# Kernel tuning notes

Hardware: AMD Instinct MI355X
Metric: run time of the kernel (lower is better)

Reference implementation:

```python
import jax, jax.numpy as jnp
import numpy as np

B, T, H, L, AS = 64, 256, 1024, 3, 128  # batch, seq-1, hidden, layers, alphabet


def setup_inputs() -> dict:
    key = jax.random.key(0)
    ks = jax.random.split(key, 8)
    # one-hot character sequence (B, T, AS), float32
    idx = jax.random.randint(ks[0], (B, T), 0, AS)
    sequence = jax.nn.one_hot(idx, AS, dtype=jnp.float32)
    u = lambda k, shape, fan: jax.random.uniform(
        k, shape, minval=-1.0 / np.sqrt(fan), maxval=1.0 / np.sqrt(fan), dtype=jnp.float32)
    W_i2h = u(ks[1], (H, AS), AS)
    b_i2h = u(ks[2], (H,), AS)
    # per-layer LSTM params, PyTorch gate order [i, f, g, o]; layer inputs all have width H
    W_ih = u(ks[3], (L, 4 * H, H), H)
    W_hh = u(ks[4], (L, 4 * H, H), H)
    b_ih = u(ks[5], (L, 4 * H), H)
    b_hh = u(ks[6], (L, 4 * H), H)
    W_h2O = u(ks[7], (AS, H), H)
    b_h2O = jnp.zeros((AS,), dtype=jnp.float32)
    h0 = jnp.zeros((L, B, H), dtype=jnp.float32)
    c0 = jnp.zeros((L, B, H), dtype=jnp.float32)
    return dict(sequence=sequence, W_i2h=W_i2h, b_i2h=b_i2h, W_ih=W_ih, W_hh=W_hh,
                b_ih=b_ih, b_hh=b_hh, W_h2O=W_h2O, b_h2O=b_h2O, h0=h0, c0=c0)


def _lstm_layer(x, h0, c0, W_ih, W_hh, b_ih, b_hh):
    # x: (B, T, H). Precompute input contribution to the gates for all steps.
    xg = jnp.einsum('bth,gh->btg', x, W_ih) + b_ih  # (B, T, 4H)

    def step(carry, xg_t):
        h, c = carry
        gates = xg_t + h @ W_hh.T + b_hh  # (B, 4H)
        i, f, g, o = jnp.split(gates, 4, axis=-1)
        c = jax.nn.sigmoid(f) * c + jax.nn.sigmoid(i) * jnp.tanh(g)
        h = jax.nn.sigmoid(o) * jnp.tanh(c)
        return (h, c), h

    (hT, cT), hs = jax.lax.scan(step, (h0, c0), jnp.swapaxes(xg, 0, 1))
    return jnp.swapaxes(hs, 0, 1), hT, cT  # (B,T,H), (B,H), (B,H)


def reference(sequence, W_i2h, b_i2h, W_ih, W_hh, b_ih, b_hh, W_h2O, b_h2O, h0, c0):
    # i2h projection
    x = jnp.einsum('bta,ha->bth', sequence, W_i2h) + b_i2h  # (B, T, H)
    # multi-layer LSTM over x (eval mode: the dropout=True arg is inactive in eval)
    inp = x
    h_fin, c_fin = [], []
    for l in range(L):
        inp, hT, cT = _lstm_layer(inp, h0[l], c0[l], W_ih[l], W_hh[l], b_ih[l], b_hh[l])
        h_fin.append(hT)
        c_fin.append(cT)
    # NOTE: faithful to the original code's bug -- h2O is applied to the i2h
    # output `x`, not to the LSTM output. The LSTM only produces the new hidden.
    out = x.reshape(-1, H) @ W_h2O.T + b_h2O  # (B*T, AS)
    return out, jnp.stack(h_fin), jnp.stack(c_fin)
```

## Files before the change

kernel.cpp:

```cpp
#include <hip/hip_runtime.h>
#include <stdint.h>
#include <stddef.h>

#define B_  64
#define T_  256
#define H_  1024
#define AS_ 128
#define L_  3

typedef __attribute__((ext_vector_type(8))) short bf16x8;
typedef __attribute__((ext_vector_type(4))) float f32x4;
typedef __attribute__((ext_vector_type(4))) unsigned u32x4;

__device__ __forceinline__ unsigned short f2bf(float f) {
  union { float f; unsigned u; } x; x.f = f;
  unsigned r = x.u + 0x7fffu + ((x.u >> 16) & 1u);
  return (unsigned short)(r >> 16);
}
__device__ __forceinline__ float bf2f(unsigned short s) {
  union { unsigned u; float f; } x; x.u = ((unsigned)s) << 16; return x.f;
}
__device__ __forceinline__ float sigmf(float x) { return 1.0f / (1.0f + __expf(-x)); }
__device__ __forceinline__ float tanh_f(float x) {
  x = fminf(fmaxf(x, -15.0f), 15.0f);
  float e = __expf(2.0f * x);
  return (e - 1.0f) / (e + 1.0f);
}

__device__ __forceinline__ void st_u16_cc(unsigned short* p, unsigned short v) {
  __hip_atomic_store(p, v, __ATOMIC_RELAXED, __HIP_MEMORY_SCOPE_AGENT);
}
__device__ __forceinline__ void st_u32_cc(unsigned* p, unsigned v) {
  __hip_atomic_store(p, v, __ATOMIC_RELAXED, __HIP_MEMORY_SCOPE_AGENT);
}
__device__ __forceinline__ unsigned ld_u32_cc(const unsigned* p) {
  return __hip_atomic_load(p, __ATOMIC_RELAXED, __HIP_MEMORY_SCOPE_AGENT);
}
__device__ __forceinline__ u32x4 ld_b128_cc_nw(const void* p) {
  u32x4 r;
  asm volatile("global_load_dwordx4 %0, %1, off sc0 sc1" : "=v"(r) : "v"(p));
  return r;
}
__device__ __forceinline__ void st_b128_cc_nw(void* p, u32x4 v) {
  asm volatile("global_store_dwordx4 %0, %1, off sc0 sc1" :: "v"(p), "v"(v) : "memory");
}
__device__ __forceinline__ void wait_vm4_tie4(u32x4& a, u32x4& b, u32x4& c, u32x4& d) {
  asm volatile("s_waitcnt vmcnt(4)"
               : "+v"(a), "+v"(b), "+v"(c), "+v"(d) :: "memory");
  __builtin_amdgcn_sched_barrier(0);
}
__device__ __forceinline__ void wait_vm0_tie4(u32x4& a, u32x4& b, u32x4& c, u32x4& d) {
  asm volatile("s_waitcnt vmcnt(0)"
               : "+v"(a), "+v"(b), "+v"(c), "+v"(d) :: "memory");
  __builtin_amdgcn_sched_barrier(0);
}
__device__ __forceinline__ void lds_barrier() {
  __builtin_amdgcn_sched_barrier(0);
  asm volatile("s_waitcnt lgkmcnt(0)" ::: "memory");
  __builtin_amdgcn_sched_barrier(0);
  __builtin_amdgcn_s_barrier();
  __builtin_amdgcn_sched_barrier(0);
}


__global__ void k_zero(unsigned* p, int n) {
  int i = blockIdx.x * 256 + threadIdx.x;
  if (i < n) st_u32_cc(p + i, 0u);
}

__global__ void k_wt_i2h(const float* __restrict__ W, const float* __restrict__ b,
                         unsigned short* __restrict__ Wt) {
  int id = blockIdx.x * 256 + threadIdx.x;
  if (id >= AS_ * H_) return;
  int a = id >> 10, h = id & 1023;
  Wt[id] = f2bf(W[h * AS_ + a] + b[h]);
}

__global__ void k_f2b(const float* __restrict__ s, unsigned short* __restrict__ d, int n) {
  int i = blockIdx.x * 256 + threadIdx.x;
  if (i < n) d[i] = f2bf(s[i]);
}

__global__ void k_bias(const float* __restrict__ bi, const float* __restrict__ bh,
                       float* __restrict__ o, int n) {
  int i = blockIdx.x * 256 + threadIdx.x;
  if (i < n) o[i] = bi[i] + bh[i];
}

__global__ __launch_bounds__(128) void k_gather(const float* __restrict__ seq,
                                                const unsigned short* __restrict__ Wt,
                                                unsigned short* __restrict__ xbf) {
  __shared__ int sidx;
  const int bt = blockIdx.x, tid = threadIdx.x;
  if (seq[(size_t)bt * AS_ + tid] > 0.5f) sidx = tid;
  __syncthreads();
  const uint4* s = (const uint4*)(Wt + (size_t)sidx * H_);
  uint4* d = (uint4*)(xbf + (size_t)bt * H_);
  d[tid] = s[tid];
}


__device__ __forceinline__ void gld16(const void* g, void* l) {
  __builtin_amdgcn_global_load_lds((const __attribute__((address_space(1))) unsigned int*)g,
                                   (__attribute__((address_space(3))) unsigned int*)l,
                                   16, 0, 0);
}

template <int OUT, int AMAJ>
__device__ __forceinline__ void gemm_tile(const unsigned short* __restrict__ A,
                                          const unsigned short* __restrict__ Bm,
                                          const float* __restrict__ bias,
                                          void* __restrict__ Cout,
                                          int m0, int n0, int K, int N, int tid,
                                          unsigned short* As, unsigned short* Bs) {
  const int lane = tid & 63, wv = tid >> 6;
  const int wr = wv >> 1, wc = wv & 1;
  const int kg = lane >> 4, li = lane & 15;
  f32x4 acc[4][4] = {};

  for (int k0 = 0; k0 < K; k0 += 32) {
    for (int i = 0; i < 2; ++i) {
      int c0 = i * 256 + wv * 64;
      int cid = c0 + lane;
      int row = cid >> 2, lc = cid & 3;
      int sc = lc ^ ((row >> 1) & 3);
      gld16(A + (size_t)(m0 + row) * K + k0 + sc * 8, (char*)As + (size_t)c0 * 16);
      gld16(Bm + (size_t)(n0 + row) * K + k0 + sc * 8, (char*)Bs + (size_t)c0 * 16);
    }
    __syncthreads();
    bf16x8 af[4], bfm[4];
#pragma unroll
    for (int mi = 0; mi < 4; ++mi) {
      int row = wr * 64 + mi * 16 + li;
      int pc = kg ^ ((row >> 1) & 3);
      af[mi] = *(const bf16x8*)((const char*)As + row * 64 + pc * 16);
    }
#pragma unroll
    for (int ni = 0; ni < 4; ++ni) {
      int row = wc * 64 + ni * 16 + li;
      int pc = kg ^ ((row >> 1) & 3);
      bfm[ni] = *(const bf16x8*)((const char*)Bs + row * 64 + pc * 16);
    }
#pragma unroll
    for (int mi = 0; mi < 4; ++mi)
#pragma unroll
      for (int ni = 0; ni < 4; ++ni)
        acc[mi][ni] = __builtin_amdgcn_mfma_f32_16x16x32_bf16(af[mi], bfm[ni], acc[mi][ni], 0, 0, 0);
    __syncthreads();
  }

#pragma unroll
  for (int mi = 0; mi < 4; ++mi)
#pragma unroll
    for (int ni = 0; ni < 4; ++ni)
#pragma unroll
      for (int r = 0; r < 4; ++r) {
        int row = m0 + wr * 64 + mi * 16 + kg * 4 + r;
        int col = n0 + wc * 64 + ni * 16 + li;
        float v = acc[mi][ni][r] + bias[col];
        if (OUT == 0) {
          ((float*)Cout)[(size_t)row * N + col] = v;
        } else {
          int b, tt;
          if (AMAJ == 0) { b = row >> 8; tt = row & 255; }
          else           { tt = row >> 6; b = row & 63; }
          int g = col >> 10, u = col & 1023;
          int idx = ((tt * 4 + (b >> 4)) << 16) | ((u >> 5) << 11) |
                    ((b & 15) << 7) | ((u & 31) << 2) | g;
          ((unsigned short*)Cout)[idx] = f2bf(v);
        }
      }
}

template <int OUT, int AMAJ>
__global__ __launch_bounds__(256) void k_gemm(const unsigned short* __restrict__ A,
                                              const unsigned short* __restrict__ Bm,
                                              const float* __restrict__ bias,
                                              void* __restrict__ Cout,
                                              int M, int N, int K) {
  __shared__ __align__(16) unsigned short As[128 * 32];
  __shared__ __align__(16) unsigned short Bs[128 * 32];
  gemm_tile<OUT, AMAJ>(A, Bm, bias, Cout, blockIdx.x * 128, blockIdx.y * 128,
                       K, N, threadIdx.x, As, Bs);
}


__global__ __launch_bounds__(256, 1) void k_fused(
    const unsigned short* __restrict__ xgs,
    const float* __restrict__ Whh,
    unsigned short* __restrict__ h_pp,
    unsigned short* __restrict__ out_seq,
    float* __restrict__ hT, float* __restrict__ cT,
    const float* __restrict__ h0, const float* __restrict__ c0,
    unsigned* __restrict__ slots,
    const unsigned short* __restrict__ WihbN,
    const float* __restrict__ bsumN,
    unsigned short* __restrict__ xgs_out) {
  __shared__ __align__(16) unsigned short Wlds[64 * 1024];
  __shared__ __align__(16) unsigned short Hs[16 * 1024];
  const int tid = threadIdx.x, lane = tid & 63, w = tid >> 6;
  const int wg = blockIdx.x;

  if (wg >= 128) {
    const int Wp = wg - 128;
    unsigned short* As = Wlds;
    unsigned short* Bs = Wlds + 4096;
    const int pline = (Wp & 31) * 32;
    for (int k = 0; k < 32; ++k) {
      const int gidx = Wp + k * 128;
      const int mt = gidx >> 5, nt = gidx & 31;
      const unsigned tgt = (unsigned)(2 * mt + 3);
      if (w == 0) {
        const unsigned* base = slots + (lane >> 4) * 1024 + pline + (lane & 15);
        unsigned v0, v1;
        do {
          __builtin_amdgcn_s_sleep(4);
          v0 = ld_u32_cc(base);
          v1 = ld_u32_cc(base + 16);
        } while (__any((int)((v0 < tgt) | (v1 < tgt))));
      }
      __syncthreads();
      gemm_tile<2, 1>(out_seq, WihbN, bsumN, (void*)xgs_out,
                      mt * 128, nt * 128, H_, 4 * H_, tid, As, Bs);
    }
    return;
  }

  const int gb = wg >> 5, ug = wg & 31;
  const int li = lane & 15, kq = lane >> 4;
  const int b  = gb * 16 + li;
  const int u0 = ug * 32 + w * 8 + kq;
  const int u1 = u0 + 4;

  st_u16_cc(&h_pp[((size_t)B_ + b) * H_ + u0], f2bf(h0[(size_t)b * H_ + u0]));
  st_u16_cc(&h_pp[((size_t)B_ + b) * H_ + u1], f2bf(h0[(size_t)b * H_ + u1]));

  bf16x8 afr[32];
  {
    const int r0 = w * 32 + li;
    const float* wr = Whh + ((size_t)(r0 & 3) * H_ + ug * 32 + (r0 >> 2)) * H_ + kq * 8;
#pragma unroll
    for (int ks = 0; ks < 32; ++ks) {
      const float4 f0 = *(const float4*)(wr + ks * 32);
      const float4 f1 = *(const float4*)(wr + ks * 32 + 4);
      union { ushort4 a[2]; bf16x8 v; } uu_;
      uu_.a[0] = ushort4{f2bf(f0.x), f2bf(f0.y), f2bf(f0.z), f2bf(f0.w)};
      uu_.a[1] = ushort4{f2bf(f1.x), f2bf(f1.y), f2bf(f1.z), f2bf(f1.w)};
      afr[ks] = uu_.v;
    }
  }
  for (int it = 0; it < 16; ++it) {
    const int r = w * 32 + 16 + it;
    const float* wr = Whh + ((size_t)(r & 3) * H_ + ug * 32 + (r >> 2)) * H_;
#pragma unroll
    for (int j = 0; j < 4; ++j) {
      const float4 f = *(const float4*)(wr + lane * 16 + j * 4);
      ushort4 p = ushort4{f2bf(f.x), f2bf(f.y), f2bf(f.z), f2bf(f.w)};
      const int k = lane * 16 + j * 4;
      *(ushort4*)((char*)Wlds + (size_t)(w * 16 + it) * 2048 + ((2 * k) ^ ((it & 7) << 4))) = p;
    }
  }
  float cs0 = c0[(size_t)b * H_ + u0], cs1 = c0[(size_t)b * H_ + u1];
  __syncthreads();
  if (w == 3 && lane < 32) {
    st_u32_cc(&slots[gb * 1024 + lane * 32 + ug], 1u);
    asm volatile("s_waitcnt vmcnt(0)" ::: "memory");
  }

  const char* hbase = (const char*)Hs + (size_t)li * 2048;
  const char* wlb   = (const char*)Wlds + (size_t)(w * 16 + li) * 2048;
  const int fxor = (li & 7) << 4;
  const int sb = tid >> 4, seg = tid & 15;
  const int sswz = (sb & 7) << 4;
  char* drow = (char*)Hs + (size_t)sb * 2048;
  unsigned short* exch = Hs;
  const unsigned* myline = slots + gb * 1024 + ug * 32;

  for (int t = 0; t < T_; ++t) {
    const size_t xb2 = ((((size_t)t * 4 + gb) << 16) | (ug << 11) | (li << 7) |
                        ((w * 8 + kq) << 2)) * 2;
    const ushort4 xa = *(const ushort4*)((const char*)xgs + xb2);
    const ushort4 xb = *(const ushort4*)((const char*)xgs + xb2 + 32);

    if (w == 0) {
      const unsigned tgt = (unsigned)(t + 1);
      unsigned v;
      do {
        __builtin_amdgcn_s_sleep(1);
        v = ld_u32_cc(&myline[lane & 31]);
      } while (__any((int)(v < tgt)));
    }
    __syncthreads();

    const char* srcrow = (const char*)(h_pp + (size_t)((t & 1) ^ 1) * (B_ * H_) +
                                       (size_t)(gb * 16 + sb) * H_);
    u32x4 A0 = ld_b128_cc_nw(srcrow +   0 * 256 + seg * 16);
    u32x4 A1 = ld_b128_cc_nw(srcrow +   1 * 256 + seg * 16);
    u32x4 A2 = ld_b128_cc_nw(srcrow +   2 * 256 + seg * 16);
    u32x4 A3 = ld_b128_cc_nw(srcrow +   3 * 256 + seg * 16);
    u32x4 B0 = ld_b128_cc_nw(srcrow + 1024 + 0 * 256 + seg * 16);
    u32x4 B1 = ld_b128_cc_nw(srcrow + 1024 + 1 * 256 + seg * 16);
    u32x4 B2 = ld_b128_cc_nw(srcrow + 1024 + 2 * 256 + seg * 16);
    u32x4 B3 = ld_b128_cc_nw(srcrow + 1024 + 3 * 256 + seg * 16);
    wait_vm4_tie4(A0, A1, A2, A3);
    *(u32x4*)(drow + ((0 * 256 + seg * 16) ^ sswz)) = A0;
    *(u32x4*)(drow + ((1 * 256 + seg * 16) ^ sswz)) = A1;
    *(u32x4*)(drow + ((2 * 256 + seg * 16) ^ sswz)) = A2;
    *(u32x4*)(drow + ((3 * 256 + seg * 16) ^ sswz)) = A3;
    lds_barrier();

    f32x4 a0 = {0.f, 0.f, 0.f, 0.f}, a1 = {0.f, 0.f, 0.f, 0.f};
#pragma unroll
    for (int ks = 0; ks < 16; ++ks) {
      const bf16x8 bb = *(const bf16x8*)(hbase + ((ks * 64 + kq * 16) ^ fxor));
      a0 = __builtin_amdgcn_mfma_f32_16x16x32_bf16(afr[ks], bb, a0, 0, 0, 0);
      const bf16x8 aw = *(const bf16x8*)(wlb + ((ks * 64 + kq * 16) ^ fxor));
      a1 = __builtin_amdgcn_mfma_f32_16x16x32_bf16(aw, bb, a1, 0, 0, 0);
    }

    wait_vm0_tie4(B0, B1, B2, B3);
    *(u32x4*)(drow + ((1024 + 0 * 256 + seg * 16) ^ sswz)) = B0;
    *(u32x4*)(drow + ((1024 + 1 * 256 + seg * 16) ^ sswz)) = B1;
    *(u32x4*)(drow + ((1024 + 2 * 256 + seg * 16) ^ sswz)) = B2;
    *(u32x4*)(drow + ((1024 + 3 * 256 + seg * 16) ^ sswz)) = B3;
    lds_barrier();

#pragma unroll
    for (int ks = 16; ks < 32; ++ks) {
      const bf16x8 bb = *(const bf16x8*)(hbase + ((ks * 64 + kq * 16) ^ fxor));
      a0 = __builtin_amdgcn_mfma_f32_16x16x32_bf16(afr[ks], bb, a0, 0, 0, 0);
      const bf16x8 aw = *(const bf16x8*)(wlb + ((ks * 64 + kq * 16) ^ fxor));
      a1 = __builtin_amdgcn_mfma_f32_16x16x32_bf16(aw, bb, a1, 0, 0, 0);
    }

    float h0v, h1v;
    {
      float gi = a0[0] + bf2f(xa.x), gf = a0[1] + bf2f(xa.y);
      float gg = a0[2] + bf2f(xa.z), go = a0[3] + bf2f(xa.w);
      float ci = sigmf(gf) * cs0 + sigmf(gi) * tanh_f(gg);
      cs0 = ci; h0v = sigmf(go) * tanh_f(ci);
    }
    {
      float gi = a1[0] + bf2f(xb.x), gf = a1[1] + bf2f(xb.y);
      float gg = a1[2] + bf2f(xb.z), go = a1[3] + bf2f(xb.w);
      float ci = sigmf(gf) * cs1 + sigmf(gi) * tanh_f(gg);
      cs1 = ci; h1v = sigmf(go) * tanh_f(ci);
    }
    const unsigned short hb0 = f2bf(h0v), hb1 = f2bf(h1v);

    __syncthreads();
    exch[li * 32 + w * 8 + kq]     = hb0;
    exch[li * 32 + w * 8 + kq + 4] = hb1;
    __syncthreads();

    if (t < T_ - 1) {
      const int bl = tid >> 4, j = tid & 15;
      const unsigned pack = (unsigned)exch[bl * 32 + 2 * j] |
                            ((unsigned)exch[bl * 32 + 2 * j + 1] << 16);
      st_u32_cc((unsigned*)&h_pp[((size_t)(t & 1) * B_ + gb * 16 + bl) * H_ + ug * 32 + 2 * j],
                pack);
    } else {
      hT[(size_t)b * H_ + u0] = h0v; hT[(size_t)b * H_ + u1] = h1v;
      cT[(size_t)b * H_ + u0] = cs0; cT[(size_t)b * H_ + u1] = cs1;
    }
    if (out_seq && tid < 64) {
      const int bo = tid >> 2, q = tid & 3;
      st_b128_cc_nw(&out_seq[((size_t)t * B_ + gb * 16 + bo) * H_ + ug * 32 + 8 * q],
                    *(const u32x4*)&exch[bo * 32 + 8 * q]);
    }
    asm volatile("s_waitcnt vmcnt(0)" ::: "memory");
    __syncthreads();
    if (w == 3 && lane < 32) {
      st_u32_cc(&slots[gb * 1024 + lane * 32 + ug], (unsigned)(t + 2));
      asm volatile("s_waitcnt vmcnt(0)" ::: "memory");
    }
  }
}


extern "C" void kernel_launch(void* const* d_in, const int* in_sizes, int n_in,
                              void* d_out, int out_size, void* d_ws, size_t ws_size,
                              hipStream_t stream) {
  const float* seq  = (const float*)d_in[0];
  const float* Wi2h = (const float*)d_in[1];
  const float* bi2h = (const float*)d_in[2];
  const float* Wih  = (const float*)d_in[3];
  const float* Whh  = (const float*)d_in[4];
  const float* bih  = (const float*)d_in[5];
  const float* bhh  = (const float*)d_in[6];
  const float* Wh2o = (const float*)d_in[7];
  const float* bh2o = (const float*)d_in[8];
  const float* h0   = (const float*)d_in[9];
  const float* c0   = (const float*)d_in[10];
  float* outF = (float*)d_out;

  size_t off = 0;
  auto nb = [&](size_t bytes) { size_t r = off; off += (bytes + 255) & ~(size_t)255; return r; };
  unsigned short* xbf   = (unsigned short*)((char*)d_ws + nb((size_t)B_ * T_ * H_ * 2));
  unsigned short* seqA  = (unsigned short*)((char*)d_ws + nb((size_t)B_ * T_ * H_ * 2));
  unsigned short* xgs   = (unsigned short*)((char*)d_ws + nb((size_t)B_ * T_ * 4 * H_ * 2));
  unsigned short* Wihb  = (unsigned short*)((char*)d_ws + nb((size_t)L_ * 4 * H_ * H_ * 2));
  unsigned short* Wh2ob = (unsigned short*)((char*)d_ws + nb((size_t)AS_ * H_ * 2));
  unsigned short* Wt    = (unsigned short*)((char*)d_ws + nb((size_t)AS_ * H_ * 2));
  float*          bsum  = (float*)((char*)d_ws + nb((size_t)L_ * 4 * H_ * 4));
  unsigned short* h_pp  = (unsigned short*)((char*)d_ws + nb((size_t)2 * B_ * H_ * 2));
  unsigned*       slt   = (unsigned*)((char*)d_ws + nb((size_t)L_ * 4 * 32 * 32 * 4));
  (void)ws_size; (void)in_sizes; (void)n_in; (void)out_size;

  const int WLAYER = 4 * H_ * H_;

  k_zero<<<(L_ * 4096 + 255) / 256, 256, 0, stream>>>(slt, L_ * 4096);
  k_wt_i2h<<<(AS_ * H_ + 255) / 256, 256, 0, stream>>>(Wi2h, bi2h, Wt);
  k_f2b<<<(L_ * WLAYER + 255) / 256, 256, 0, stream>>>(Wih, Wihb, L_ * WLAYER);
  k_f2b<<<(AS_ * H_ + 255) / 256, 256, 0, stream>>>(Wh2o, Wh2ob, AS_ * H_);
  k_bias<<<(L_ * 4 * H_ + 255) / 256, 256, 0, stream>>>(bih, bhh, bsum, L_ * 4 * H_);
  k_gather<<<B_ * T_, 128, 0, stream>>>(seq, Wt, xbf);

  k_gemm<0, 0><<<dim3(B_ * T_ / 128, AS_ / 128), 256, 0, stream>>>(
      xbf, Wh2ob, bh2o, (void*)outF, B_ * T_, AS_, H_);

  k_gemm<2, 0><<<dim3(B_ * T_ / 128, 4 * H_ / 128), 256, 0, stream>>>(
      xbf, Wihb, bsum, (void*)xgs, B_ * T_, 4 * H_, H_);

  float* hT_base = outF + (size_t)B_ * T_ * AS_;
  float* cT_base = hT_base + (size_t)L_ * B_ * H_;

  k_fused<<<256, 256, 0, stream>>>(
      xgs, Whh, h_pp, seqA,
      hT_base, cT_base, h0, c0, slt,
      Wihb + (size_t)1 * WLAYER, bsum + (size_t)1 * 4 * H_, xgs);

  k_fused<<<256, 256, 0, stream>>>(
      xgs, Whh + (size_t)1 * WLAYER, h_pp, xbf,
      hT_base + (size_t)B_ * H_, cT_base + (size_t)B_ * H_,
      h0 + (size_t)B_ * H_, c0 + (size_t)B_ * H_, slt + (size_t)4096,
      Wihb + (size_t)2 * WLAYER, bsum + (size_t)2 * 4 * H_, xgs);

  k_fused<<<128, 256, 0, stream>>>(
      xgs, Whh + (size_t)2 * WLAYER, h_pp, nullptr,
      hT_base + (size_t)2 * B_ * H_, cT_base + (size_t)2 * B_ * H_,
      h0 + (size_t)2 * B_ * H_, c0 + (size_t)2 * B_ * H_, slt + (size_t)2 * 4096,
      nullptr, nullptr, nullptr);
}
```

Measured before the change: 3.488 ms.

## Fold layer-0 input GEMM and output projection into fused recurrent kernel with progress flags

The standalone layer-0 input-projection GEMM and the h2O output GEMM are removed and run inside the first fused LSTM kernel's spare worker blocks. Those blocks publish per-tile progress counters, and the recurrent blocks poll them before reading each timestep's gate inputs. The gather writes x in time-major order to match, and five small prep kernels are merged into one launch. The aim is to overlap the big input GEMM with the sequential recurrence and cut launch overhead. In exchange it adds polling cost, coherent loads on the gate-input path, and a risk of contention between the GEMM blocks and the recurrent ones.

```diff
diff --git a/kernel.cpp b/kernel.cpp
--- a/kernel.cpp
+++ b/kernel.cpp
@@ -41,12 +41,18 @@
   asm volatile("global_load_dwordx4 %0, %1, off sc0 sc1" : "=v"(r) : "v"(p));
   return r;
 }
+__device__ __forceinline__ unsigned long long ld_b64_cc_nw(const void* p) {
+  unsigned long long r;
+  asm volatile("global_load_dwordx2 %0, %1, off sc0 sc1" : "=v"(r) : "v"(p));
+  return r;
+}
 __device__ __forceinline__ void st_b128_cc_nw(void* p, u32x4 v) {
   asm volatile("global_store_dwordx4 %0, %1, off sc0 sc1" :: "v"(p), "v"(v) : "memory");
 }
-__device__ __forceinline__ void wait_vm4_tie4(u32x4& a, u32x4& b, u32x4& c, u32x4& d) {
+__device__ __forceinline__ void wait_vm4_tie6(u32x4& a, u32x4& b, u32x4& c, u32x4& d,
+                                              unsigned long long& x, unsigned long long& y) {
   asm volatile("s_waitcnt vmcnt(4)"
-               : "+v"(a), "+v"(b), "+v"(c), "+v"(d) :: "memory");
+               : "+v"(a), "+v"(b), "+v"(c), "+v"(d), "+v"(x), "+v"(y) :: "memory");
   __builtin_amdgcn_sched_barrier(0);
 }
 __device__ __forceinline__ void wait_vm0_tie4(u32x4& a, u32x4& b, u32x4& c, u32x4& d) {
@@ -63,28 +69,23 @@
 }
 
 
-__global__ void k_zero(unsigned* p, int n) {
+__global__ void k_prep(unsigned* __restrict__ zp, int nzero,
+                       const float* __restrict__ Wi2h, const float* __restrict__ bi2h,
+                       unsigned short* __restrict__ Wt,
+                       const float* __restrict__ Wih, unsigned short* __restrict__ Wihb, int nwih,
+                       const float* __restrict__ Wh2o, unsigned short* __restrict__ Wh2ob,
+                       const float* __restrict__ bih, const float* __restrict__ bhh,
+                       float* __restrict__ bsum) {
   int i = blockIdx.x * 256 + threadIdx.x;
-  if (i < n) st_u32_cc(p + i, 0u);
-}
-
-__global__ void k_wt_i2h(const float* __restrict__ W, const float* __restrict__ b,
-                         unsigned short* __restrict__ Wt) {
-  int id = blockIdx.x * 256 + threadIdx.x;
-  if (id >= AS_ * H_) return;
-  int a = id >> 10, h = id & 1023;
-  Wt[id] = f2bf(W[h * AS_ + a] + b[h]);
-}
-
-__global__ void k_f2b(const float* __restrict__ s, unsigned short* __restrict__ d, int n) {
-  int i = blockIdx.x * 256 + threadIdx.x;
-  if (i < n) d[i] = f2bf(s[i]);
-}
-
-__global__ void k_bias(const float* __restrict__ bi, const float* __restrict__ bh,
-                       float* __restrict__ o, int n) {
-  int i = blockIdx.x * 256 + threadIdx.x;
-  if (i < n) o[i] = bi[i] + bh[i];
+  if (i < nzero) { st_u32_cc(zp + i, 0u); return; }
+  i -= nzero;
+  if (i < AS_ * H_) { int a = i >> 10, h = i & 1023; Wt[i] = f2bf(Wi2h[h * AS_ + a] + bi2h[h]); return; }
+  i -= AS_ * H_;
+  if (i < nwih) { Wihb[i] = f2bf(Wih[i]); return; }
+  i -= nwih;
+  if (i < AS_ * H_) { Wh2ob[i] = f2bf(Wh2o[i]); return; }
+  i -= AS_ * H_;
+  if (i < L_ * 4 * H_) bsum[i] = bih[i] + bhh[i];
 }
 
 __global__ __launch_bounds__(128) void k_gather(const float* __restrict__ seq,
@@ -94,8 +95,9 @@
   const int bt = blockIdx.x, tid = threadIdx.x;
   if (seq[(size_t)bt * AS_ + tid] > 0.5f) sidx = tid;
   __syncthreads();
+  const int b = bt >> 8, t = bt & 255;
   const uint4* s = (const uint4*)(Wt + (size_t)sidx * H_);
-  uint4* d = (uint4*)(xbf + (size_t)bt * H_);
+  uint4* d = (uint4*)(xbf + ((size_t)t * B_ + b) * H_);
   d[tid] = s[tid];
 }
 
@@ -106,7 +108,7 @@
                                    16, 0, 0);
 }
 
-template <int OUT, int AMAJ>
+template <int OUT>
 __device__ __forceinline__ void gemm_tile(const unsigned short* __restrict__ A,
                                           const unsigned short* __restrict__ Bm,
                                           const float* __restrict__ bias,
@@ -158,30 +160,17 @@
         int row = m0 + wr * 64 + mi * 16 + kg * 4 + r;
         int col = n0 + wc * 64 + ni * 16 + li;
         float v = acc[mi][ni][r] + bias[col];
-        if (OUT == 0) {
-          ((float*)Cout)[(size_t)row * N + col] = v;
+        int tt = row >> 6, b = row & 63;
+        if (OUT == 4) {
+          ((float*)Cout)[(size_t)(b * 256 + tt) * N + col] = v;
         } else {
-          int b, tt;
-          if (AMAJ == 0) { b = row >> 8; tt = row & 255; }
-          else           { tt = row >> 6; b = row & 63; }
           int g = col >> 10, u = col & 1023;
           int idx = ((tt * 4 + (b >> 4)) << 16) | ((u >> 5) << 11) |
                     ((b & 15) << 7) | ((u & 31) << 2) | g;
-          ((unsigned short*)Cout)[idx] = f2bf(v);
+          if (OUT == 3) st_u16_cc(&((unsigned short*)Cout)[idx], f2bf(v));
+          else          ((unsigned short*)Cout)[idx] = f2bf(v);
         }
       }
-}
-
-template <int OUT, int AMAJ>
-__global__ __launch_bounds__(256) void k_gemm(const unsigned short* __restrict__ A,
-                                              const unsigned short* __restrict__ Bm,
-                                              const float* __restrict__ bias,
-                                              void* __restrict__ Cout,
-                                              int M, int N, int K) {
-  __shared__ __align__(16) unsigned short As[128 * 32];
-  __shared__ __align__(16) unsigned short Bs[128 * 32];
-  gemm_tile<OUT, AMAJ>(A, Bm, bias, Cout, blockIdx.x * 128, blockIdx.y * 128,
-                       K, N, threadIdx.x, As, Bs);
 }
 
 
@@ -195,7 +184,14 @@
     unsigned* __restrict__ slots,
     const unsigned short* __restrict__ WihbN,
     const float* __restrict__ bsumN,
-    unsigned short* __restrict__ xgs_out) {
+    unsigned short* __restrict__ xgs_out,
+    const unsigned short* __restrict__ xg0A,
+    const unsigned short* __restrict__ Wihb0,
+    const float* __restrict__ bsum0,
+    unsigned* __restrict__ xgprog,
+    const unsigned short* __restrict__ WoutB,
+    const float* __restrict__ bout,
+    float* __restrict__ outC) {
   __shared__ __align__(16) unsigned short Wlds[64 * 1024];
   __shared__ __align__(16) unsigned short Hs[16 * 1024];
   const int tid = threadIdx.x, lane = tid & 63, w = tid >> 6;
@@ -205,23 +201,39 @@
     const int Wp = wg - 128;
     unsigned short* As = Wlds;
     unsigned short* Bs = Wlds + 4096;
-    const int pline = (Wp & 31) * 32;
-    for (int k = 0; k < 32; ++k) {
-      const int gidx = Wp + k * 128;
-      const int mt = gidx >> 5, nt = gidx & 31;
-      const unsigned tgt = (unsigned)(2 * mt + 3);
-      if (w == 0) {
-        const unsigned* base = slots + (lane >> 4) * 1024 + pline + (lane & 15);
-        unsigned v0, v1;
-        do {
-          __builtin_amdgcn_s_sleep(4);
-          v0 = ld_u32_cc(base);
-          v1 = ld_u32_cc(base + 16);
-        } while (__any((int)((v0 < tgt) | (v1 < tgt))));
+    if (xg0A) {
+      for (int k = 0; k < 32; ++k) {
+        const int gidx = k * 128 + Wp;
+        gemm_tile<3>(xg0A, Wihb0, bsum0, (void*)xgs_out,
+                     (gidx >> 5) * 128, (gidx & 31) * 128, H_, 4 * H_, tid, As, Bs);
+        asm volatile("s_waitcnt vmcnt(0)" ::: "memory");
+        __syncthreads();
+        if (tid == 0) {
+          st_u32_cc(&xgprog[Wp], (unsigned)(k + 1));
+          asm volatile("s_waitcnt vmcnt(0)" ::: "memory");
+        }
       }
-      __syncthreads();
-      gemm_tile<2, 1>(out_seq, WihbN, bsumN, (void*)xgs_out,
-                      mt * 128, nt * 128, H_, 4 * H_, tid, As, Bs);
+      gemm_tile<4>(xg0A, WoutB, bout, (void*)outC, Wp * 128, 0, H_, AS_, tid, As, Bs);
+    }
+    if (WihbN) {
+      const int pline = (Wp & 31) * 32;
+      for (int k = 0; k < 32; ++k) {
+        const int gidx = Wp + k * 128;
+        const int mt = gidx >> 5, nt = gidx & 31;
+        const unsigned tgt = (unsigned)(2 * mt + 3);
+        if (w == 0) {
+          const unsigned* base = slots + (lane >> 4) * 1024 + pline + (lane & 15);
+          unsigned v0, v1;
+          do {
+            __builtin_amdgcn_s_sleep(4);
+            v0 = ld_u32_cc(base);
+            v1 = ld_u32_cc(base + 16);
+          } while (__any((int)((v0 < tgt) | (v1 < tgt))));
+        }
+        __syncthreads();
+        gemm_tile<2>(out_seq, WihbN, bsumN, (void*)xgs_out,
+                     mt * 128, nt * 128, H_, 4 * H_, tid, As, Bs);
+      }
     }
     return;
   }
@@ -277,21 +289,24 @@
   const unsigned* myline = slots + gb * 1024 + ug * 32;
 
   for (int t = 0; t < T_; ++t) {
-    const size_t xb2 = ((((size_t)t * 4 + gb) << 16) | (ug << 11) | (li << 7) |
-                        ((w * 8 + kq) << 2)) * 2;
-    const ushort4 xa = *(const ushort4*)((const char*)xgs + xb2);
-    const ushort4 xb = *(const ushort4*)((const char*)xgs + xb2 + 32);
-
     if (w == 0) {
       const unsigned tgt = (unsigned)(t + 1);
-      unsigned v;
+      const int mt = t >> 1;
+      const unsigned gtgt = (unsigned)((mt >> 2) + 1);
+      const unsigned* gp = xgprog ? (xgprog + (mt & 3) * 32 + (lane & 31)) : nullptr;
+      unsigned v, g;
       do {
         __builtin_amdgcn_s_sleep(1);
         v = ld_u32_cc(&myline[lane & 31]);
-      } while (__any((int)(v < tgt)));
-    }
-    __syncthreads();
-
+        g = gp ? ld_u32_cc(gp) : 0x7FFFFFFFu;
+      } while (__any((int)((v < tgt) | (g < gtgt))));
+    }
+    __syncthreads();
+
+    const size_t xb2 = ((((size_t)t * 4 + gb) << 16) | (ug << 11) | (li << 7) |
+                        ((w * 8 + kq) << 2)) * 2;
+    unsigned long long xar = ld_b64_cc_nw((const char*)xgs + xb2);
+    unsigned long long xbr = ld_b64_cc_nw((const char*)xgs + xb2 + 32);
     const char* srcrow = (const char*)(h_pp + (size_t)((t & 1) ^ 1) * (B_ * H_) +
                                        (size_t)(gb * 16 + sb) * H_);
     u32x4 A0 = ld_b128_cc_nw(srcrow +   0 * 256 + seg * 16);
@@ -302,7 +317,7 @@
     u32x4 B1 = ld_b128_cc_nw(srcrow + 1024 + 1 * 256 + seg * 16);
     u32x4 B2 = ld_b128_cc_nw(srcrow + 1024 + 2 * 256 + seg * 16);
     u32x4 B3 = ld_b128_cc_nw(srcrow + 1024 + 3 * 256 + seg * 16);
-    wait_vm4_tie4(A0, A1, A2, A3);
+    wait_vm4_tie6(A0, A1, A2, A3, xar, xbr);
     *(u32x4*)(drow + ((0 * 256 + seg * 16) ^ sswz)) = A0;
     *(u32x4*)(drow + ((1 * 256 + seg * 16) ^ sswz)) = A1;
     *(u32x4*)(drow + ((2 * 256 + seg * 16) ^ sswz)) = A2;
@@ -333,6 +348,8 @@
       a1 = __builtin_amdgcn_mfma_f32_16x16x32_bf16(aw, bb, a1, 0, 0, 0);
     }
 
+    const ushort4 xa = *(const ushort4*)&xar;
+    const ushort4 xb = *(const ushort4*)&xbr;
     float h0v, h1v;
     {
       float gi = a0[0] + bf2f(xa.x), gf = a0[1] + bf2f(xa.y);
@@ -404,23 +421,17 @@
   unsigned short* Wt    = (unsigned short*)((char*)d_ws + nb((size_t)AS_ * H_ * 2));
   float*          bsum  = (float*)((char*)d_ws + nb((size_t)L_ * 4 * H_ * 4));
   unsigned short* h_pp  = (unsigned short*)((char*)d_ws + nb((size_t)2 * B_ * H_ * 2));
-  unsigned*       slt   = (unsigned*)((char*)d_ws + nb((size_t)L_ * 4 * 32 * 32 * 4));
+  unsigned*       slt   = (unsigned*)((char*)d_ws + nb((size_t)(L_ * 4096 + 128) * 4));
+  unsigned*       xgp   = slt + L_ * 4096;
   (void)ws_size; (void)in_sizes; (void)n_in; (void)out_size;
 
   const int WLAYER = 4 * H_ * H_;
-
-  k_zero<<<(L_ * 4096 + 255) / 256, 256, 0, stream>>>(slt, L_ * 4096);
-  k_wt_i2h<<<(AS_ * H_ + 255) / 256, 256, 0, stream>>>(Wi2h, bi2h, Wt);
-  k_f2b<<<(L_ * WLAYER + 255) / 256, 256, 0, stream>>>(Wih, Wihb, L_ * WLAYER);
-  k_f2b<<<(AS_ * H_ + 255) / 256, 256, 0, stream>>>(Wh2o, Wh2ob, AS_ * H_);
-  k_bias<<<(L_ * 4 * H_ + 255) / 256, 256, 0, stream>>>(bih, bhh, bsum, L_ * 4 * H_);
+  const int nzero = L_ * 4096 + 128;
+  const int nprep = nzero + 2 * AS_ * H_ + L_ * WLAYER + L_ * 4 * H_;
+
+  k_prep<<<(nprep + 255) / 256, 256, 0, stream>>>(
+      slt, nzero, Wi2h, bi2h, Wt, Wih, Wihb, L_ * WLAYER, Wh2o, Wh2ob, bih, bhh, bsum);
   k_gather<<<B_ * T_, 128, 0, stream>>>(seq, Wt, xbf);
-
-  k_gemm<0, 0><<<dim3(B_ * T_ / 128, AS_ / 128), 256, 0, stream>>>(
-      xbf, Wh2ob, bh2o, (void*)outF, B_ * T_, AS_, H_);
-
-  k_gemm<2, 0><<<dim3(B_ * T_ / 128, 4 * H_ / 128), 256, 0, stream>>>(
-      xbf, Wihb, bsum, (void*)xgs, B_ * T_, 4 * H_, H_);
 
   float* hT_base = outF + (size_t)B_ * T_ * AS_;
   float* cT_base = hT_base + (size_t)L_ * B_ * H_;
@@ -428,17 +439,19 @@
   k_fused<<<256, 256, 0, stream>>>(
       xgs, Whh, h_pp, seqA,
       hT_base, cT_base, h0, c0, slt,
-      Wihb + (size_t)1 * WLAYER, bsum + (size_t)1 * 4 * H_, xgs);
+      Wihb + (size_t)1 * WLAYER, bsum + (size_t)1 * 4 * H_, xgs,
+      xbf, Wihb, bsum, xgp, Wh2ob, bh2o, outF);
 
   k_fused<<<256, 256, 0, stream>>>(
       xgs, Whh + (size_t)1 * WLAYER, h_pp, xbf,
       hT_base + (size_t)B_ * H_, cT_base + (size_t)B_ * H_,
       h0 + (size_t)B_ * H_, c0 + (size_t)B_ * H_, slt + (size_t)4096,
-      Wihb + (size_t)2 * WLAYER, bsum + (size_t)2 * 4 * H_, xgs);
+      Wihb + (size_t)2 * WLAYER, bsum + (size_t)2 * 4 * H_, xgs,
+      nullptr, nullptr, nullptr, nullptr, nullptr, nullptr, nullptr);
 
   k_fused<<<128, 256, 0, stream>>>(
       xgs, Whh + (size_t)2 * WLAYER, h_pp, nullptr,
       hT_base + (size_t)2 * B_ * H_, cT_base + (size_t)2 * B_ * H_,
       h0 + (size_t)2 * B_ * H_, c0 + (size_t)2 * B_ * H_, slt + (size_t)2 * 4096,
-      nullptr, nullptr, nullptr);
-}
+      nullptr, nullptr, nullptr, nullptr, nullptr, nullptr, nullptr, nullptr, nullptr, nullptr);
+}
```

After: 3.538 ms. No clear change (+1.4%).
